# Optimization experiments

Hardware: AMD Instinct MI355X
Metric: run time of the kernel (lower is better)

Reference implementation:

```python
import jax, jax.numpy as jnp
import numpy as np

H = 132  # hidden size hard-coded in SpatialRelationLayer

def _mlp(x, w1, b1, w2, b2, w3, b3):
    # FCBlock: 2 hidden layers of width 132 with ReLU, then linear out;
    # NNNet wraps it with sigmoid(out * 5)
    h = jax.nn.relu(x @ w1 + b1)
    h = jax.nn.relu(h @ w2 + b2)
    return jax.nn.sigmoid((h @ w3 + b3) * 5.0)

def _mlp_params(key, din, dout):
    k1, k2, k3 = jax.random.split(key, 3)
    def lin(k, i, o):
        kw, kb = jax.random.split(k)
        s = 1.0 / np.sqrt(i)
        return (jax.random.uniform(kw, (i, o), jnp.float32, -s, s),
                jax.random.uniform(kb, (o,), jnp.float32, -s, s))
    w1, b1 = lin(k1, din, H)
    w2, b2 = lin(k2, H, H)
    w3, b3 = lin(k3, H, dout)
    return w1, b1, w2, b2, w3, b3

def setup_inputs() -> dict:
    key = jax.random.key(0)
    b, N, D0, D1, D2 = 8, 128, 128, 128, 64
    O0, O1, O2 = 64, 64, 64
    kP, kQ, kR, kp, kq, kr = jax.random.split(key, 6)
    inp = {
        "P": jax.random.normal(kP, (b, D0), jnp.float32),
        "Q": jax.random.normal(kQ, (b, N, D1), jnp.float32),
        "R": jax.random.normal(kR, (b, N, N, D2), jnp.float32),
    }
    for name, k, din, dout in (("p", kp, D0 + D1, O0),
                               ("q", kq, D1 + D0 + 2 * D2, O1),
                               ("r", kr, D2 + 2 * D1, O2)):
        w1, b1, w2, b2, w3, b3 = _mlp_params(k, din, dout)
        inp.update({f"{name}_w1": w1, f"{name}_b1": b1,
                    f"{name}_w2": w2, f"{name}_b2": b2,
                    f"{name}_w3": w3, f"{name}_b3": b3})
    return inp

def reference(P, Q, R,
              p_w1, p_b1, p_w2, p_b2, p_w3, p_b3,
              q_w1, q_b1, q_w2, q_b2, q_w3, q_b3,
              r_w1, r_b1, r_w2, r_b2, r_w3, r_b3):
    b, N, D1 = Q.shape
    # P branch: global max over objects, concat with P
    P_inputs = jnp.concatenate([jnp.max(Q, axis=1), P], axis=1)  # [b, D1+D0]
    P_out = _mlp(P_inputs, p_w1, p_b1, p_w2, p_b2, p_w3, p_b3)
    # Q branch: broadcast P per-object, max-reduce relations over each axis
    P_exp = jnp.broadcast_to(P[:, None, :], (b, N, P.shape[1]))  # [b,N,D0]
    R_red0 = jnp.max(R, axis=1)  # [b,N,D2]
    R_red1 = jnp.max(R, axis=2)  # [b,N,D2]
    Q_inputs = jnp.concatenate([P_exp, Q, R_red0, R_red1], axis=2)
    Q_out = _mlp(Q_inputs, q_w1, q_b1, q_w2, q_b2, q_w3, q_b3)
    # R branch: pairwise broadcast of Q along both axes, concat with R
    Q0 = jnp.broadcast_to(Q[:, None, :, :], (b, N, N, D1))  # repeat along dim 1
    Q1 = jnp.broadcast_to(Q[:, :, None, :], (b, N, N, D1))  # repeat along dim 2
    R_inputs = jnp.concatenate([R, Q0, Q1], axis=-1)  # [b,N,N,D2+2*D1]
    R_out = _mlp(R_inputs, r_w1, r_b1, r_w2, r_b2, r_w3, r_b3)
    return (P_out, Q_out, R_out)
```

## Files before the change

kernel.cpp:

```cpp
#include <hip/hip_runtime.h>

typedef _Float16 f16;
typedef f16 f16x8 __attribute__((ext_vector_type(8)));
typedef f16 f16x4 __attribute__((ext_vector_type(4)));
typedef float f32x4 __attribute__((ext_vector_type(4)));
typedef float f32x2 __attribute__((ext_vector_type(2)));

#define MFMA16(a, b, c) __builtin_amdgcn_mfma_f32_16x16x32_f16(a, b, c, 0, 0, 0)

#define OFF_RW1A 0
#define OFF_RW2  10240
#define OFF_RW3  35840
#define OFF_QW1  46080
#define OFF_QW2  87040
#define OFF_QW3  112640
#define OFF_PW1  122880
#define OFF_PW2  163840
#define OFF_PW3  189440
#define PACK_BYTES 399360

#define PREP_BLOCKS 1523

struct InPtrs { const float* p[21]; };

__device__ const int g_mSrc[9] = {15, 17, 19, 9, 11, 13, 3, 5, 7};
__device__ const int g_mK0[9]  = {0, 0, 0, 128, 0, 0, 0, 0, 0};
__device__ const int g_mK[9]   = {64, 132, 132, 256, 132, 132, 256, 132, 132};
__device__ const int g_mN[9]   = {132, 132, 64, 132, 132, 64, 132, 132, 64};
__device__ const int g_mNT[9]  = {10, 10, 4, 10, 10, 4, 10, 10, 4};
__device__ const int g_mDst[9] = {OFF_RW1A, OFF_RW2, OFF_RW3, OFF_QW1, OFF_QW2, OFF_QW3,
                                  OFF_PW1, OFF_PW2, OFF_PW3};
__device__ const int g_mBlk0[9] = {128, 133, 146, 151, 171, 184, 189, 209, 222};

__global__ __launch_bounds__(256) void prep_kernel(InPtrs in, f16* __restrict__ wpk,
    float* __restrict__ c1, float* __restrict__ d1, float* __restrict__ e1q,
    float* __restrict__ qmax, float* __restrict__ red0, float* __restrict__ red1)
{
  __shared__ float sbuf[1024];
  const int mb = blockIdx.x, t = threadIdx.x;

  if (mb < 128) {
    const int b = mb >> 4, jo = mb & 15;
    const float* base = in.p[2] + (size_t)b * 1048576 + (size_t)jo * 512 + t * 2;
    f32x2 m[8];
    #pragma unroll
    for (int u = 0; u < 8; ++u) { m[u][0] = -3.4e38f; m[u][1] = -3.4e38f; }
    for (int i = 0; i < 128; i += 8) {
      #pragma unroll
      for (int u = 0; u < 8; ++u) {
        f32x2 v = *(const f32x2*)(base + (size_t)(i + u) * 8192);
        m[u][0] = fmaxf(m[u][0], v[0]);
        m[u][1] = fmaxf(m[u][1], v[1]);
      }
    }
    #pragma unroll
    for (int s = 4; s > 0; s >>= 1)
      #pragma unroll
      for (int u = 0; u < 4; ++u)
        if (u < s) {
          m[u][0] = fmaxf(m[u][0], m[u + s][0]);
          m[u][1] = fmaxf(m[u][1], m[u + s][1]);
        }
    *(f32x2*)(red0 + ((size_t)(b * 128 + jo * 8 + (t >> 5))) * 64 + ((t * 2) & 63)) = m[0];
  } else if (mb < 227) {
    int mi = 8;
    while (mi > 0 && mb < g_mBlk0[mi]) --mi;
    const int NT = g_mNT[mi], K = g_mK[mi], N = g_mN[mi], K0 = g_mK0[mi];
    const int L = (mb - g_mBlk0[mi]) * 256 + t;
    const int lanes = ((K + 31) >> 5) * NT * 64;
    if (L < lanes) {
      const int lane = L & 63, tile = L >> 6;
      const int kk = tile / NT, nn = tile % NT;
      const float* src = in.p[g_mSrc[mi]];
      const int n = nn * 16 + (lane & 15);
      const int kb = kk * 32 + ((lane >> 4) << 3);
      f16x8 v;
      #pragma unroll
      for (int u = 0; u < 8; ++u) {
        const int k = kb + u;
        float f = (k < K && n < N) ? src[(size_t)(K0 + k) * N + n] : 0.f;
        v[u] = (f16)f;
      }
      *(f16x8*)(wpk + g_mDst[mi] + (size_t)L * 8) = v;
    }
  } else if (mb < 235) {
    const int b = mb - 227;
    const float* Qb = in.p[1] + (size_t)b * 128 * 128;
    const int d = t & 127, g = t >> 7;
    float m0 = -3.4e38f, m1 = m0, m2 = m0, m3 = m0;
    #pragma unroll
    for (int v = 0; v < 16; ++v) {
      const int i = g * 64 + v * 4;
      m0 = fmaxf(m0, Qb[(size_t)(i + 0) * 128 + d]);
      m1 = fmaxf(m1, Qb[(size_t)(i + 1) * 128 + d]);
      m2 = fmaxf(m2, Qb[(size_t)(i + 2) * 128 + d]);
      m3 = fmaxf(m3, Qb[(size_t)(i + 3) * 128 + d]);
    }
    sbuf[g * 128 + d] = fmaxf(fmaxf(m0, m1), fmaxf(m2, m3));
    __syncthreads();
    if (t < 128) qmax[b * 128 + t] = fmaxf(sbuf[t], sbuf[128 + t]);
  } else if (mb < 243) {
    const int b = mb - 235;
    const float* P = in.p[0]; const float* qw1 = in.p[9]; const float* qb1 = in.p[10];
    if (t < 160) {
      float a = 0.f;
      if (t < 132) {
        float a0 = 0.f, a1 = 0.f, a2 = 0.f, a3 = 0.f;
        for (int k = 0; k < 128; k += 4) {
          a0 += P[b * 128 + k + 0] * qw1[(size_t)(k + 0) * 132 + t];
          a1 += P[b * 128 + k + 1] * qw1[(size_t)(k + 1) * 132 + t];
          a2 += P[b * 128 + k + 2] * qw1[(size_t)(k + 2) * 132 + t];
          a3 += P[b * 128 + k + 3] * qw1[(size_t)(k + 3) * 132 + t];
        }
        a = qb1[t] + (a0 + a1) + (a2 + a3);
      }
      e1q[b * 160 + t] = a;
    }
  } else if (mb < 499) {
    const int blk = mb - 243;
    const float* Q = in.p[1]; const float* rw1 = in.p[15]; const float* rb1 = in.p[16];
    for (int o = t; o < 512; o += 256) sbuf[o] = Q[(size_t)blk * 512 + o];
    __syncthreads();
    if (t < 160) {
      float cc[4], dd[4];
      #pragma unroll
      for (int r = 0; r < 4; ++r) { cc[r] = 0.f; dd[r] = 0.f; }
      if (t < 132) {
        const float bb = rb1[t];
        #pragma unroll
        for (int r = 0; r < 4; ++r) cc[r] = bb;
        for (int k = 0; k < 128; ++k) {
          const float wc = rw1[(size_t)(192 + k) * 132 + t];
          const float wd = rw1[(size_t)(64 + k) * 132 + t];
          #pragma unroll
          for (int r = 0; r < 4; ++r) {
            cc[r] += sbuf[r * 128 + k] * wc;
            dd[r] += sbuf[r * 128 + k] * wd;
          }
        }
      }
      for (int r = 0; r < 4; ++r) {
        c1[(size_t)(blk * 4 + r) * 160 + t] = cc[r];
        d1[(size_t)(blk * 4 + r) * 160 + t] = dd[r];
      }
    }
  } else {
    const int bi = mb - 499;
    const int d2 = t & 31, jg = t >> 5;
    const float* base = in.p[2] + (size_t)bi * 8192 + (size_t)jg * 1024 + d2 * 2;
    f32x2 m[4];
    #pragma unroll
    for (int u = 0; u < 4; ++u) { m[u][0] = -3.4e38f; m[u][1] = -3.4e38f; }
    #pragma unroll
    for (int v = 0; v < 16; v += 4) {
      #pragma unroll
      for (int u = 0; u < 4; ++u) {
        f32x2 vv = *(const f32x2*)(base + (size_t)(v + u) * 64);
        m[u][0] = fmaxf(m[u][0], vv[0]);
        m[u][1] = fmaxf(m[u][1], vv[1]);
      }
    }
    m[0][0] = fmaxf(fmaxf(m[0][0], m[1][0]), fmaxf(m[2][0], m[3][0]));
    m[0][1] = fmaxf(fmaxf(m[0][1], m[1][1]), fmaxf(m[2][1], m[3][1]));
    sbuf[jg * 64 + d2 * 2] = m[0][0];
    sbuf[jg * 64 + d2 * 2 + 1] = m[0][1];
    __syncthreads();
    if (t < 64) {
      float mm = sbuf[t];
      #pragma unroll
      for (int g2 = 1; g2 < 8; ++g2) mm = fmaxf(mm, sbuf[g2 * 64 + t]);
      red1[(size_t)bi * 64 + t] = mm;
    }
  }
}

__device__ __forceinline__ float sig5(float x) {
  return 1.f / (1.f + __expf(-5.f * x));
}

__device__ __forceinline__ f16x8 ld_frag_f32(const float* p) {
  f32x4 v0 = *(const f32x4*)(p);
  f32x4 v1 = *(const f32x4*)(p + 4);
  f16x8 a;
  a[0] = (f16)v0[0]; a[1] = (f16)v0[1]; a[2] = (f16)v0[2]; a[3] = (f16)v0[3];
  a[4] = (f16)v1[0]; a[5] = (f16)v1[1]; a[6] = (f16)v1[2]; a[7] = (f16)v1[3];
  return a;
}

__global__ __launch_bounds__(256, 4) void fused_kernel(
    const float* __restrict__ R, const float* __restrict__ c1, const float* __restrict__ d1,
    const float* __restrict__ rb2, const float* __restrict__ rb3,
    const f16* __restrict__ wpk, float* __restrict__ outR,
    const float* __restrict__ P, const float* __restrict__ Q,
    const float* __restrict__ qb2, const float* __restrict__ qb3,
    const float* __restrict__ pb1, const float* __restrict__ pb2, const float* __restrict__ pb3,
    const float* __restrict__ e1q, const float* __restrict__ qmax,
    const float* __restrict__ red0, const float* __restrict__ red1,
    float* __restrict__ outP, float* __restrict__ outQ)
{
  __shared__ f16 Hs[64][168];
  const int blk = blockIdx.x;
  const int t = threadIdx.x, lane = t & 63, w = t >> 6;
  const int wm = w >> 1, wn = w & 1;
  const int lr = (lane >> 4) << 2;
  const int lc = lane & 15;
  const int lk = (lane >> 4) << 3;
  const int rbase = wm * 32, nbase = wn * 80;

  f32x4 acc[2][5];
  const float* b2p;
  const float* b3p;
  const f16x8* W2p;
  const f16x8* W3p;
  float* obase;
  int rowlim;

  if (blk >= 17) {
    const int idx = blk - 17;
    const int bi = idx >> 1, half = idx & 1;
    const int jbase = half * 64;
    const int b = bi >> 7;
    const float* Rb = R + (size_t)bi * 8192 + (size_t)jbase * 64;

    const float* c1r = c1 + (size_t)bi * 160;
    const float* d1b = d1 + ((size_t)b * 128 + jbase) * 160;
    f32x4 cvv[5];
    #pragma unroll
    for (int n5 = 0; n5 < 5; ++n5)
      cvv[n5] = *(const f32x4*)(c1r + nbase + n5 * 16 + lr);
    #pragma unroll
    for (int mi2 = 0; mi2 < 2; ++mi2) {
      const int jl = rbase + mi2 * 16 + lc;
      const float* dr = d1b + (size_t)jl * 160 + nbase + lr;
      #pragma unroll
      for (int n5 = 0; n5 < 5; ++n5)
        acc[mi2][n5] = cvv[n5] + *(const f32x4*)(dr + n5 * 16);
    }
    const f16x8* W1p = (const f16x8*)(wpk + OFF_RW1A);
    #pragma unroll
    for (int kk = 0; kk < 2; ++kk) {
      const f16x8 a0 = ld_frag_f32(Rb + (size_t)(rbase + lc) * 64 + kk * 32 + lk);
      const f16x8 a1 = ld_frag_f32(Rb + (size_t)(rbase + 16 + lc) * 64 + kk * 32 + lk);
      #pragma unroll
      for (int n5 = 0; n5 < 5; ++n5) {
        const f16x8 bf = W1p[(size_t)(kk * 10 + wn * 5 + n5) * 64 + lane];
        acc[0][n5] = MFMA16(bf, a0, acc[0][n5]);
        acc[1][n5] = MFMA16(bf, a1, acc[1][n5]);
      }
    }
    b2p = rb2; b3p = rb3;
    W2p = (const f16x8*)(wpk + OFF_RW2);
    W3p = (const f16x8*)(wpk + OFF_RW3);
    obase = outR + (size_t)bi * 8192 + (size_t)jbase * 64;
    rowlim = 64;
  } else {
    const int bs = blk;
    const bool isP = (bs == 16);
    const int b = bs >> 1, x0 = (bs & 1) * 64;
    const f16x8* W1p = (const f16x8*)(wpk + (isP ? OFF_PW1 : OFF_QW1));
    const f16x8 zz = {0, 0, 0, 0, 0, 0, 0, 0};

    #pragma unroll
    for (int n5 = 0; n5 < 5; ++n5) {
      const int nb = nbase + n5 * 16 + lr;
      f32x4 cv = {0.f, 0.f, 0.f, 0.f};
      if (isP) { if (nb < 132) cv = *(const f32x4*)(pb1 + nb); }
      else cv = *(const f32x4*)(e1q + b * 160 + nb);
      acc[0][n5] = cv; acc[1][n5] = cv;
    }
    for (int c = 0; c < 4; ++c) {
      #pragma unroll
      for (int kk = 0; kk < 2; ++kk) {
        const int kq = c * 64 + kk * 32 + lk;
        f16x8 a0 = zz, a1 = zz;
        if (isP) {
          #pragma unroll
          for (int mi2 = 0; mi2 < 2; ++mi2) {
            const int rl = rbase + mi2 * 16 + lc;
            f16x8 av = zz;
            if (rl < 8) {
              const float* s = (c < 2) ? (qmax + rl * 128 + kq) : (P + rl * 128 + (kq - 128));
              av = ld_frag_f32(s);
            }
            if (mi2 == 0) a0 = av; else a1 = av;
          }
        } else {
          #pragma unroll
          for (int mi2 = 0; mi2 < 2; ++mi2) {
            const size_t rg = (size_t)(b * 128 + x0 + rbase + mi2 * 16 + lc);
            const float* s = (c < 2) ? (Q + rg * 128 + kq)
                           : ((kq < 192) ? (red0 + rg * 64 + (kq - 128))
                                         : (red1 + rg * 64 + (kq - 192)));
            const f16x8 av = ld_frag_f32(s);
            if (mi2 == 0) a0 = av; else a1 = av;
          }
        }
        #pragma unroll
        for (int n5 = 0; n5 < 5; ++n5) {
          const f16x8 bf = W1p[(size_t)((c * 2 + kk) * 10 + wn * 5 + n5) * 64 + lane];
          acc[0][n5] = MFMA16(bf, a0, acc[0][n5]);
          acc[1][n5] = MFMA16(bf, a1, acc[1][n5]);
        }
      }
    }
    b2p = isP ? pb2 : qb2; b3p = isP ? pb3 : qb3;
    W2p = (const f16x8*)(wpk + (isP ? OFF_PW2 : OFF_QW2));
    W3p = (const f16x8*)(wpk + (isP ? OFF_PW3 : OFF_QW3));
    obase = isP ? outP : (outQ + ((size_t)(b * 128 + x0)) * 64);
    rowlim = isP ? 8 : 64;
  }

  #pragma unroll
  for (int mi2 = 0; mi2 < 2; ++mi2) {
    const int jl = rbase + mi2 * 16 + lc;
    #pragma unroll
    for (int n5 = 0; n5 < 5; ++n5) {
      f16x4 hv;
      #pragma unroll
      for (int r = 0; r < 4; ++r) hv[r] = (f16)fmaxf(acc[mi2][n5][r], 0.f);
      *(f16x4*)(&Hs[jl][nbase + n5 * 16 + lr]) = hv;
    }
  }
  __syncthreads();

  #pragma unroll
  for (int n5 = 0; n5 < 5; ++n5) {
    const int nb = nbase + n5 * 16 + lr;
    f32x4 bv = {0.f, 0.f, 0.f, 0.f};
    if (nb < 132) bv = *(const f32x4*)(b2p + nb);
    acc[0][n5] = bv; acc[1][n5] = bv;
  }
  #pragma unroll
  for (int kk = 0; kk < 5; ++kk) {
    const f16x8 a0 = *(const f16x8*)(&Hs[rbase + lc][kk * 32 + lk]);
    const f16x8 a1 = *(const f16x8*)(&Hs[rbase + 16 + lc][kk * 32 + lk]);
    #pragma unroll
    for (int n5 = 0; n5 < 5; ++n5) {
      const f16x8 bf = W2p[(size_t)(kk * 10 + wn * 5 + n5) * 64 + lane];
      acc[0][n5] = MFMA16(bf, a0, acc[0][n5]);
      acc[1][n5] = MFMA16(bf, a1, acc[1][n5]);
    }
  }
  __syncthreads();
  #pragma unroll
  for (int mi2 = 0; mi2 < 2; ++mi2) {
    const int jl = rbase + mi2 * 16 + lc;
    #pragma unroll
    for (int n5 = 0; n5 < 5; ++n5) {
      f16x4 hv;
      #pragma unroll
      for (int r = 0; r < 4; ++r) hv[r] = (f16)fmaxf(acc[mi2][n5][r], 0.f);
      *(f16x4*)(&Hs[jl][nbase + n5 * 16 + lr]) = hv;
    }
  }
  __syncthreads();

  f32x4 acc3[2][2];
  const int n3base = wn * 32;
  #pragma unroll
  for (int n2 = 0; n2 < 2; ++n2) {
    const f32x4 bv = *(const f32x4*)(b3p + n3base + n2 * 16 + lr);
    acc3[0][n2] = bv; acc3[1][n2] = bv;
  }
  #pragma unroll
  for (int kk = 0; kk < 5; ++kk) {
    const f16x8 a0 = *(const f16x8*)(&Hs[rbase + lc][kk * 32 + lk]);
    const f16x8 a1 = *(const f16x8*)(&Hs[rbase + 16 + lc][kk * 32 + lk]);
    #pragma unroll
    for (int n2 = 0; n2 < 2; ++n2) {
      const f16x8 bf = W3p[(size_t)(kk * 4 + wn * 2 + n2) * 64 + lane];
      acc3[0][n2] = MFMA16(bf, a0, acc3[0][n2]);
      acc3[1][n2] = MFMA16(bf, a1, acc3[1][n2]);
    }
  }
  #pragma unroll
  for (int mi2 = 0; mi2 < 2; ++mi2) {
    const int jl = rbase + mi2 * 16 + lc;
    if (jl < rowlim) {
      #pragma unroll
      for (int n2 = 0; n2 < 2; ++n2) {
        f32x4 ov;
        #pragma unroll
        for (int r = 0; r < 4; ++r) ov[r] = sig5(acc3[mi2][n2][r]);
        *(f32x4*)(obase + (size_t)jl * 64 + n3base + n2 * 16 + lr) = ov;
      }
    }
  }
}

extern "C" void kernel_launch(void* const* d_in, const int* in_sizes, int n_in,
                              void* d_out, int out_size, void* d_ws, size_t ws_size,
                              hipStream_t stream) {
  (void)in_sizes; (void)n_in; (void)out_size; (void)ws_size;
  InPtrs ip;
  for (int i = 0; i < 21; ++i) ip.p[i] = (const float*)d_in[i];

  char* ws = (char*)d_ws;
  f16* wpk = (f16*)ws;
  float* wsf = (float*)(ws + PACK_BYTES);
  float* c1 = wsf;
  float* d1 = wsf + 163840;
  float* e1q = wsf + 327680;
  float* qmax = wsf + 328960;
  float* red0 = wsf + 329984;
  float* red1 = wsf + 395520;

  float* outP = (float*)d_out;
  float* outQ = outP + 512;
  float* outR = outP + 66048;

  prep_kernel<<<dim3(PREP_BLOCKS), dim3(256), 0, stream>>>(ip, wpk, c1, d1, e1q, qmax, red0, red1);
  fused_kernel<<<dim3(2065), dim3(256), 0, stream>>>((const float*)d_in[2], c1, d1,
      (const float*)d_in[18], (const float*)d_in[20], wpk, outR,
      (const float*)d_in[0], (const float*)d_in[1],
      (const float*)d_in[12], (const float*)d_in[14],
      (const float*)d_in[4], (const float*)d_in[6], (const float*)d_in[8],
      e1q, qmax, red0, red1, outP, outQ);
}
```

Measured before the change: 64.46 us.

## Make each wave own full MLP rows and pass hidden layers via lane shuffles

The fused MLP kernel now gives each wave 32 rows across all 132 hidden columns, so layer outputs are repacked into MFMA operand fragments with cross-lane shuffles instead of going through shared memory and __syncthreads. It also uses packed round-to-zero f16 conversion, splits the R max-over-axis-1 reduction into two halves combined in the Q branch, and relaxes launch bounds to 3 blocks. The aim is to remove LDS traffic and block barriers and to add parallelism to the column reduction. In exchange, register pressure rises from doubled accumulators and there are extra shuffle instructions.

```diff
diff --git a/kernel.cpp b/kernel.cpp
--- a/kernel.cpp
+++ b/kernel.cpp
@@ -2,9 +2,9 @@
 
 typedef _Float16 f16;
 typedef f16 f16x8 __attribute__((ext_vector_type(8)));
-typedef f16 f16x4 __attribute__((ext_vector_type(4)));
 typedef float f32x4 __attribute__((ext_vector_type(4)));
 typedef float f32x2 __attribute__((ext_vector_type(2)));
+typedef unsigned u32;
 
 #define MFMA16(a, b, c) __builtin_amdgcn_mfma_f32_16x16x32_f16(a, b, c, 0, 0, 0)
 
@@ -19,7 +19,7 @@
 #define OFF_PW3  189440
 #define PACK_BYTES 399360
 
-#define PREP_BLOCKS 1523
+#define PREP_BLOCKS 1651
 
 struct InPtrs { const float* p[21]; };
 
@@ -30,22 +30,23 @@
 __device__ const int g_mNT[9]  = {10, 10, 4, 10, 10, 4, 10, 10, 4};
 __device__ const int g_mDst[9] = {OFF_RW1A, OFF_RW2, OFF_RW3, OFF_QW1, OFF_QW2, OFF_QW3,
                                   OFF_PW1, OFF_PW2, OFF_PW3};
-__device__ const int g_mBlk0[9] = {128, 133, 146, 151, 171, 184, 189, 209, 222};
+__device__ const int g_mBlk0[9] = {256, 261, 274, 279, 299, 312, 317, 337, 350};
 
 __global__ __launch_bounds__(256) void prep_kernel(InPtrs in, f16* __restrict__ wpk,
     float* __restrict__ c1, float* __restrict__ d1, float* __restrict__ e1q,
-    float* __restrict__ qmax, float* __restrict__ red0, float* __restrict__ red1)
+    float* __restrict__ qmax, float* __restrict__ red0p, float* __restrict__ red1)
 {
   __shared__ float sbuf[1024];
   const int mb = blockIdx.x, t = threadIdx.x;
 
-  if (mb < 128) {
-    const int b = mb >> 4, jo = mb & 15;
-    const float* base = in.p[2] + (size_t)b * 1048576 + (size_t)jo * 512 + t * 2;
+  if (mb < 256) {
+    const int b = mb >> 5, jo = (mb >> 1) & 15, ih = mb & 1;
+    const float* base = in.p[2] + (size_t)b * 1048576 + (size_t)ih * 64 * 8192
+                        + (size_t)jo * 512 + t * 2;
     f32x2 m[8];
     #pragma unroll
     for (int u = 0; u < 8; ++u) { m[u][0] = -3.4e38f; m[u][1] = -3.4e38f; }
-    for (int i = 0; i < 128; i += 8) {
+    for (int i = 0; i < 64; i += 8) {
       #pragma unroll
       for (int u = 0; u < 8; ++u) {
         f32x2 v = *(const f32x2*)(base + (size_t)(i + u) * 8192);
@@ -61,8 +62,9 @@
           m[u][0] = fmaxf(m[u][0], m[u + s][0]);
           m[u][1] = fmaxf(m[u][1], m[u + s][1]);
         }
-    *(f32x2*)(red0 + ((size_t)(b * 128 + jo * 8 + (t >> 5))) * 64 + ((t * 2) & 63)) = m[0];
-  } else if (mb < 227) {
+    *(f32x2*)(red0p + (size_t)ih * 65536 +
+              ((size_t)(b * 128 + jo * 8 + (t >> 5))) * 64 + ((t * 2) & 63)) = m[0];
+  } else if (mb < 355) {
     int mi = 8;
     while (mi > 0 && mb < g_mBlk0[mi]) --mi;
     const int NT = g_mNT[mi], K = g_mK[mi], N = g_mN[mi], K0 = g_mK0[mi];
@@ -83,8 +85,8 @@
       }
       *(f16x8*)(wpk + g_mDst[mi] + (size_t)L * 8) = v;
     }
-  } else if (mb < 235) {
-    const int b = mb - 227;
+  } else if (mb < 363) {
+    const int b = mb - 355;
     const float* Qb = in.p[1] + (size_t)b * 128 * 128;
     const int d = t & 127, g = t >> 7;
     float m0 = -3.4e38f, m1 = m0, m2 = m0, m3 = m0;
@@ -99,8 +101,8 @@
     sbuf[g * 128 + d] = fmaxf(fmaxf(m0, m1), fmaxf(m2, m3));
     __syncthreads();
     if (t < 128) qmax[b * 128 + t] = fmaxf(sbuf[t], sbuf[128 + t]);
-  } else if (mb < 243) {
-    const int b = mb - 235;
+  } else if (mb < 371) {
+    const int b = mb - 363;
     const float* P = in.p[0]; const float* qw1 = in.p[9]; const float* qb1 = in.p[10];
     if (t < 160) {
       float a = 0.f;
@@ -116,8 +118,8 @@
       }
       e1q[b * 160 + t] = a;
     }
-  } else if (mb < 499) {
-    const int blk = mb - 243;
+  } else if (mb < 627) {
+    const int blk = mb - 371;
     const float* Q = in.p[1]; const float* rw1 = in.p[15]; const float* rb1 = in.p[16];
     for (int o = t; o < 512; o += 256) sbuf[o] = Q[(size_t)blk * 512 + o];
     __syncthreads();
@@ -145,7 +147,7 @@
       }
     }
   } else {
-    const int bi = mb - 499;
+    const int bi = mb - 627;
     const int d2 = t & 31, jg = t >> 5;
     const float* base = in.p[2] + (size_t)bi * 8192 + (size_t)jg * 1024 + d2 * 2;
     f32x2 m[4];
@@ -178,16 +180,51 @@
   return 1.f / (1.f + __expf(-5.f * x));
 }
 
-__device__ __forceinline__ f16x8 ld_frag_f32(const float* p) {
-  f32x4 v0 = *(const f32x4*)(p);
-  f32x4 v1 = *(const f32x4*)(p + 4);
-  f16x8 a;
-  a[0] = (f16)v0[0]; a[1] = (f16)v0[1]; a[2] = (f16)v0[2]; a[3] = (f16)v0[3];
-  a[4] = (f16)v1[0]; a[5] = (f16)v1[1]; a[6] = (f16)v1[2]; a[7] = (f16)v1[3];
-  return a;
-}
-
-__global__ __launch_bounds__(256, 4) void fused_kernel(
+__device__ __forceinline__ u32 pk2(float a, float b) {
+  typedef __fp16 fp16x2 __attribute__((ext_vector_type(2)));
+  union { fp16x2 h; u32 u; } cv;
+  cv.h = __builtin_amdgcn_cvt_pkrtz(a, b);
+  return cv.u;
+}
+
+__device__ __forceinline__ f16x8 ld8(const float* p) {
+  f32x4 v0 = *(const f32x4*)p, v1 = *(const f32x4*)(p + 4);
+  union { u32 w[4]; f16x8 v; } U;
+  U.w[0] = pk2(v0[0], v0[1]); U.w[1] = pk2(v0[2], v0[3]);
+  U.w[2] = pk2(v1[0], v1[1]); U.w[3] = pk2(v1[2], v1[3]);
+  return U.v;
+}
+
+__device__ __forceinline__ f16x8 ld8max(const float* p, int stride) {
+  f32x4 a0 = *(const f32x4*)p, a1 = *(const f32x4*)(p + 4);
+  f32x4 b0 = *(const f32x4*)(p + stride), b1 = *(const f32x4*)(p + stride + 4);
+  union { u32 w[4]; f16x8 v; } U;
+  U.w[0] = pk2(fmaxf(a0[0], b0[0]), fmaxf(a0[1], b0[1]));
+  U.w[1] = pk2(fmaxf(a0[2], b0[2]), fmaxf(a0[3], b0[3]));
+  U.w[2] = pk2(fmaxf(a1[0], b1[0]), fmaxf(a1[1], b1[1]));
+  U.w[3] = pk2(fmaxf(a1[2], b1[2]), fmaxf(a1[3], b1[3]));
+  return U.v;
+}
+
+__device__ __forceinline__ f16x8 make_bfrag(const f32x4 ta, const f32x4 tb,
+                                            int srcA, int srcB, bool glo) {
+  u32 a0 = pk2(fmaxf(ta[0], 0.f), fmaxf(ta[1], 0.f));
+  u32 a1 = pk2(fmaxf(ta[2], 0.f), fmaxf(ta[3], 0.f));
+  u32 b0 = pk2(fmaxf(tb[0], 0.f), fmaxf(tb[1], 0.f));
+  u32 b1 = pk2(fmaxf(tb[2], 0.f), fmaxf(tb[3], 0.f));
+  u32 aA0 = (u32)__shfl((int)a0, srcA), aA1 = (u32)__shfl((int)a1, srcA);
+  u32 bA0 = (u32)__shfl((int)b0, srcA), bA1 = (u32)__shfl((int)b1, srcA);
+  u32 aB0 = (u32)__shfl((int)a0, srcB), aB1 = (u32)__shfl((int)a1, srcB);
+  u32 bB0 = (u32)__shfl((int)b0, srcB), bB1 = (u32)__shfl((int)b1, srcB);
+  union { u32 w[4]; f16x8 v; } U;
+  U.w[0] = glo ? aA0 : bA0;
+  U.w[1] = glo ? aA1 : bA1;
+  U.w[2] = glo ? aB0 : bB0;
+  U.w[3] = glo ? aB1 : bB1;
+  return U.v;
+}
+
+__global__ __launch_bounds__(256, 3) void fused_kernel(
     const float* __restrict__ R, const float* __restrict__ c1, const float* __restrict__ d1,
     const float* __restrict__ rb2, const float* __restrict__ rb3,
     const f16* __restrict__ wpk, float* __restrict__ outR,
@@ -195,194 +232,170 @@
     const float* __restrict__ qb2, const float* __restrict__ qb3,
     const float* __restrict__ pb1, const float* __restrict__ pb2, const float* __restrict__ pb3,
     const float* __restrict__ e1q, const float* __restrict__ qmax,
-    const float* __restrict__ red0, const float* __restrict__ red1,
+    const float* __restrict__ red0p, const float* __restrict__ red1,
     float* __restrict__ outP, float* __restrict__ outQ)
 {
-  __shared__ f16 Hs[64][168];
-  const int blk = blockIdx.x;
   const int t = threadIdx.x, lane = t & 63, w = t >> 6;
-  const int wm = w >> 1, wn = w & 1;
-  const int lr = (lane >> 4) << 2;
-  const int lc = lane & 15;
-  const int lk = (lane >> 4) << 3;
-  const int rbase = wm * 32, nbase = wn * 80;
-
-  f32x4 acc[2][5];
-  const float* b2p;
-  const float* b3p;
-  const f16x8* W2p;
-  const f16x8* W3p;
+  const int g = lane >> 4, i = lane & 15;
+  const int nrow = g * 4;
+  const bool glo = (g < 2);
+  const int srcA = ((2 * g) & 3) * 16 + i;
+  const int srcB = ((2 * g + 1) & 3) * 16 + i;
+  const int wv = blockIdx.x * 4 + w;
+  if (wv >= 4129) return;
+
+  f32x4 acc[2][10];
+  const f16x8 *W2p, *W3p;
+  const float *b2p, *b3p;
   float* obase;
   int rowlim;
 
-  if (blk >= 17) {
-    const int idx = blk - 17;
-    const int bi = idx >> 1, half = idx & 1;
-    const int jbase = half * 64;
+  if (wv >= 33) {
+    const int widx = wv - 33;
+    const int bi = widx >> 2, rowbase = (widx & 3) * 32;
     const int b = bi >> 7;
-    const float* Rb = R + (size_t)bi * 8192 + (size_t)jbase * 64;
-
     const float* c1r = c1 + (size_t)bi * 160;
-    const float* d1b = d1 + ((size_t)b * 128 + jbase) * 160;
-    f32x4 cvv[5];
-    #pragma unroll
-    for (int n5 = 0; n5 < 5; ++n5)
-      cvv[n5] = *(const f32x4*)(c1r + nbase + n5 * 16 + lr);
-    #pragma unroll
-    for (int mi2 = 0; mi2 < 2; ++mi2) {
-      const int jl = rbase + mi2 * 16 + lc;
-      const float* dr = d1b + (size_t)jl * 160 + nbase + lr;
-      #pragma unroll
-      for (int n5 = 0; n5 < 5; ++n5)
-        acc[mi2][n5] = cvv[n5] + *(const f32x4*)(dr + n5 * 16);
+    const float* d1b = d1 + ((size_t)(b * 128 + rowbase)) * 160;
+    #pragma unroll
+    for (int tn = 0; tn < 10; ++tn) {
+      const f32x4 cv = *(const f32x4*)(c1r + tn * 16 + nrow);
+      #pragma unroll
+      for (int tj = 0; tj < 2; ++tj)
+        acc[tj][tn] = cv + *(const f32x4*)(d1b + (size_t)(tj * 16 + i) * 160 + tn * 16 + nrow);
     }
     const f16x8* W1p = (const f16x8*)(wpk + OFF_RW1A);
-    #pragma unroll
-    for (int kk = 0; kk < 2; ++kk) {
-      const f16x8 a0 = ld_frag_f32(Rb + (size_t)(rbase + lc) * 64 + kk * 32 + lk);
-      const f16x8 a1 = ld_frag_f32(Rb + (size_t)(rbase + 16 + lc) * 64 + kk * 32 + lk);
-      #pragma unroll
-      for (int n5 = 0; n5 < 5; ++n5) {
-        const f16x8 bf = W1p[(size_t)(kk * 10 + wn * 5 + n5) * 64 + lane];
-        acc[0][n5] = MFMA16(bf, a0, acc[0][n5]);
-        acc[1][n5] = MFMA16(bf, a1, acc[1][n5]);
-      }
-    }
+    const float* Rb = R + (size_t)bi * 8192 + (size_t)rowbase * 64;
+    #pragma unroll
+    for (int c = 0; c < 2; ++c) {
+      const f16x8 x0 = ld8(Rb + (size_t)i * 64 + c * 32 + g * 8);
+      const f16x8 x1 = ld8(Rb + (size_t)(16 + i) * 64 + c * 32 + g * 8);
+      #pragma unroll
+      for (int tn = 0; tn < 10; ++tn) {
+        const f16x8 bf = W1p[(size_t)(c * 10 + tn) * 64 + lane];
+        acc[0][tn] = MFMA16(bf, x0, acc[0][tn]);
+        acc[1][tn] = MFMA16(bf, x1, acc[1][tn]);
+      }
+    }
+    W2p = (const f16x8*)(wpk + OFF_RW2); W3p = (const f16x8*)(wpk + OFF_RW3);
     b2p = rb2; b3p = rb3;
-    W2p = (const f16x8*)(wpk + OFF_RW2);
-    W3p = (const f16x8*)(wpk + OFF_RW3);
-    obase = outR + (size_t)bi * 8192 + (size_t)jbase * 64;
-    rowlim = 64;
+    obase = outR + (size_t)bi * 8192 + (size_t)rowbase * 64;
+    rowlim = 32;
+  } else if (wv < 32) {
+    const int b = wv >> 2, rowbase = (wv & 3) * 32;
+    const int rgb = b * 128 + rowbase;
+    #pragma unroll
+    for (int tn = 0; tn < 10; ++tn) {
+      const f32x4 ev = *(const f32x4*)(e1q + b * 160 + tn * 16 + nrow);
+      acc[0][tn] = ev; acc[1][tn] = ev;
+    }
+    const f16x8* W1p = (const f16x8*)(wpk + OFF_QW1);
+    #pragma unroll
+    for (int c = 0; c < 8; ++c) {
+      f16x8 x[2];
+      #pragma unroll
+      for (int tj = 0; tj < 2; ++tj) {
+        const size_t row = (size_t)(rgb + tj * 16 + i);
+        if (c < 4)      x[tj] = ld8(Q + row * 128 + c * 32 + g * 8);
+        else if (c < 6) x[tj] = ld8max(red0p + row * 64 + (c - 4) * 32 + g * 8, 65536);
+        else            x[tj] = ld8(red1 + row * 64 + (c - 6) * 32 + g * 8);
+      }
+      #pragma unroll
+      for (int tn = 0; tn < 10; ++tn) {
+        const f16x8 bf = W1p[(size_t)(c * 10 + tn) * 64 + lane];
+        acc[0][tn] = MFMA16(bf, x[0], acc[0][tn]);
+        acc[1][tn] = MFMA16(bf, x[1], acc[1][tn]);
+      }
+    }
+    W2p = (const f16x8*)(wpk + OFF_QW2); W3p = (const f16x8*)(wpk + OFF_QW3);
+    b2p = qb2; b3p = qb3;
+    obase = outQ + (size_t)rgb * 64;
+    rowlim = 32;
   } else {
-    const int bs = blk;
-    const bool isP = (bs == 16);
-    const int b = bs >> 1, x0 = (bs & 1) * 64;
-    const f16x8* W1p = (const f16x8*)(wpk + (isP ? OFF_PW1 : OFF_QW1));
-    const f16x8 zz = {0, 0, 0, 0, 0, 0, 0, 0};
-
-    #pragma unroll
-    for (int n5 = 0; n5 < 5; ++n5) {
-      const int nb = nbase + n5 * 16 + lr;
+    #pragma unroll
+    for (int tn = 0; tn < 10; ++tn) {
+      const int nb = tn * 16 + nrow;
       f32x4 cv = {0.f, 0.f, 0.f, 0.f};
-      if (isP) { if (nb < 132) cv = *(const f32x4*)(pb1 + nb); }
-      else cv = *(const f32x4*)(e1q + b * 160 + nb);
-      acc[0][n5] = cv; acc[1][n5] = cv;
-    }
-    for (int c = 0; c < 4; ++c) {
-      #pragma unroll
-      for (int kk = 0; kk < 2; ++kk) {
-        const int kq = c * 64 + kk * 32 + lk;
-        f16x8 a0 = zz, a1 = zz;
-        if (isP) {
-          #pragma unroll
-          for (int mi2 = 0; mi2 < 2; ++mi2) {
-            const int rl = rbase + mi2 * 16 + lc;
-            f16x8 av = zz;
-            if (rl < 8) {
-              const float* s = (c < 2) ? (qmax + rl * 128 + kq) : (P + rl * 128 + (kq - 128));
-              av = ld_frag_f32(s);
-            }
-            if (mi2 == 0) a0 = av; else a1 = av;
-          }
-        } else {
-          #pragma unroll
-          for (int mi2 = 0; mi2 < 2; ++mi2) {
-            const size_t rg = (size_t)(b * 128 + x0 + rbase + mi2 * 16 + lc);
-            const float* s = (c < 2) ? (Q + rg * 128 + kq)
-                           : ((kq < 192) ? (red0 + rg * 64 + (kq - 128))
-                                         : (red1 + rg * 64 + (kq - 192)));
-            const f16x8 av = ld_frag_f32(s);
-            if (mi2 == 0) a0 = av; else a1 = av;
-          }
-        }
-        #pragma unroll
-        for (int n5 = 0; n5 < 5; ++n5) {
-          const f16x8 bf = W1p[(size_t)((c * 2 + kk) * 10 + wn * 5 + n5) * 64 + lane];
-          acc[0][n5] = MFMA16(bf, a0, acc[0][n5]);
-          acc[1][n5] = MFMA16(bf, a1, acc[1][n5]);
-        }
-      }
-    }
-    b2p = isP ? pb2 : qb2; b3p = isP ? pb3 : qb3;
-    W2p = (const f16x8*)(wpk + (isP ? OFF_PW2 : OFF_QW2));
-    W3p = (const f16x8*)(wpk + (isP ? OFF_PW3 : OFF_QW3));
-    obase = isP ? outP : (outQ + ((size_t)(b * 128 + x0)) * 64);
-    rowlim = isP ? 8 : 64;
+      if (nb < 132) cv = *(const f32x4*)(pb1 + nb);
+      acc[0][tn] = cv; acc[1][tn] = cv;
+    }
+    const f16x8* W1p = (const f16x8*)(wpk + OFF_PW1);
+    #pragma unroll
+    for (int c = 0; c < 8; ++c) {
+      f16x8 x[2];
+      #pragma unroll
+      for (int tj = 0; tj < 2; ++tj) {
+        const int rr = (tj * 16 + i) & 7;
+        const float* s = (c < 4) ? (qmax + rr * 128 + c * 32 + g * 8)
+                                 : (P + rr * 128 + (c - 4) * 32 + g * 8);
+        x[tj] = ld8(s);
+      }
+      #pragma unroll
+      for (int tn = 0; tn < 10; ++tn) {
+        const f16x8 bf = W1p[(size_t)(c * 10 + tn) * 64 + lane];
+        acc[0][tn] = MFMA16(bf, x[0], acc[0][tn]);
+        acc[1][tn] = MFMA16(bf, x[1], acc[1][tn]);
+      }
+    }
+    W2p = (const f16x8*)(wpk + OFF_PW2); W3p = (const f16x8*)(wpk + OFF_PW3);
+    b2p = pb2; b3p = pb3;
+    obase = outP;
+    rowlim = 8;
   }
 
-  #pragma unroll
-  for (int mi2 = 0; mi2 < 2; ++mi2) {
-    const int jl = rbase + mi2 * 16 + lc;
-    #pragma unroll
-    for (int n5 = 0; n5 < 5; ++n5) {
-      f16x4 hv;
-      #pragma unroll
-      for (int r = 0; r < 4; ++r) hv[r] = (f16)fmaxf(acc[mi2][n5][r], 0.f);
-      *(f16x4*)(&Hs[jl][nbase + n5 * 16 + lr]) = hv;
-    }
-  }
-  __syncthreads();
-
-  #pragma unroll
-  for (int n5 = 0; n5 < 5; ++n5) {
-    const int nb = nbase + n5 * 16 + lr;
+  f16x8 hf[5][2];
+  #pragma unroll
+  for (int c = 0; c < 5; ++c)
+    #pragma unroll
+    for (int tj = 0; tj < 2; ++tj)
+      hf[c][tj] = make_bfrag(acc[tj][2 * c], acc[tj][2 * c + 1], srcA, srcB, glo);
+
+  #pragma unroll
+  for (int tn = 0; tn < 10; ++tn) {
+    const int nb = tn * 16 + nrow;
     f32x4 bv = {0.f, 0.f, 0.f, 0.f};
     if (nb < 132) bv = *(const f32x4*)(b2p + nb);
-    acc[0][n5] = bv; acc[1][n5] = bv;
+    acc[0][tn] = bv; acc[1][tn] = bv;
   }
   #pragma unroll
-  for (int kk = 0; kk < 5; ++kk) {
-    const f16x8 a0 = *(const f16x8*)(&Hs[rbase + lc][kk * 32 + lk]);
-    const f16x8 a1 = *(const f16x8*)(&Hs[rbase + 16 + lc][kk * 32 + lk]);
-    #pragma unroll
-    for (int n5 = 0; n5 < 5; ++n5) {
-      const f16x8 bf = W2p[(size_t)(kk * 10 + wn * 5 + n5) * 64 + lane];
-      acc[0][n5] = MFMA16(bf, a0, acc[0][n5]);
-      acc[1][n5] = MFMA16(bf, a1, acc[1][n5]);
-    }
+  for (int c = 0; c < 5; ++c)
+    #pragma unroll
+    for (int tn = 0; tn < 10; ++tn) {
+      const f16x8 bf = W2p[(size_t)(c * 10 + tn) * 64 + lane];
+      acc[0][tn] = MFMA16(bf, hf[c][0], acc[0][tn]);
+      acc[1][tn] = MFMA16(bf, hf[c][1], acc[1][tn]);
+    }
+
+  #pragma unroll
+  for (int c = 0; c < 5; ++c)
+    #pragma unroll
+    for (int tj = 0; tj < 2; ++tj)
+      hf[c][tj] = make_bfrag(acc[tj][2 * c], acc[tj][2 * c + 1], srcA, srcB, glo);
+
+  f32x4 a3[2][4];
+  #pragma unroll
+  for (int tn = 0; tn < 4; ++tn) {
+    const f32x4 bv = *(const f32x4*)(b3p + tn * 16 + nrow);
+    a3[0][tn] = bv; a3[1][tn] = bv;
   }
-  __syncthreads();
-  #pragma unroll
-  for (int mi2 = 0; mi2 < 2; ++mi2) {
-    const int jl = rbase + mi2 * 16 + lc;
-    #pragma unroll
-    for (int n5 = 0; n5 < 5; ++n5) {
-      f16x4 hv;
-      #pragma unroll
-      for (int r = 0; r < 4; ++r) hv[r] = (f16)fmaxf(acc[mi2][n5][r], 0.f);
-      *(f16x4*)(&Hs[jl][nbase + n5 * 16 + lr]) = hv;
-    }
-  }
-  __syncthreads();
-
-  f32x4 acc3[2][2];
-  const int n3base = wn * 32;
-  #pragma unroll
-  for (int n2 = 0; n2 < 2; ++n2) {
-    const f32x4 bv = *(const f32x4*)(b3p + n3base + n2 * 16 + lr);
-    acc3[0][n2] = bv; acc3[1][n2] = bv;
-  }
-  #pragma unroll
-  for (int kk = 0; kk < 5; ++kk) {
-    const f16x8 a0 = *(const f16x8*)(&Hs[rbase + lc][kk * 32 + lk]);
-    const f16x8 a1 = *(const f16x8*)(&Hs[rbase + 16 + lc][kk * 32 + lk]);
-    #pragma unroll
-    for (int n2 = 0; n2 < 2; ++n2) {
-      const f16x8 bf = W3p[(size_t)(kk * 4 + wn * 2 + n2) * 64 + lane];
-      acc3[0][n2] = MFMA16(bf, a0, acc3[0][n2]);
-      acc3[1][n2] = MFMA16(bf, a1, acc3[1][n2]);
-    }
-  }
-  #pragma unroll
-  for (int mi2 = 0; mi2 < 2; ++mi2) {
-    const int jl = rbase + mi2 * 16 + lc;
-    if (jl < rowlim) {
-      #pragma unroll
-      for (int n2 = 0; n2 < 2; ++n2) {
+  #pragma unroll
+  for (int c = 0; c < 5; ++c)
+    #pragma unroll
+    for (int tn = 0; tn < 4; ++tn) {
+      const f16x8 bf = W3p[(size_t)(c * 4 + tn) * 64 + lane];
+      a3[0][tn] = MFMA16(bf, hf[c][0], a3[0][tn]);
+      a3[1][tn] = MFMA16(bf, hf[c][1], a3[1][tn]);
+    }
+
+  #pragma unroll
+  for (int tj = 0; tj < 2; ++tj) {
+    const int jr = tj * 16 + i;
+    if (jr < rowlim) {
+      #pragma unroll
+      for (int tn = 0; tn < 4; ++tn) {
         f32x4 ov;
         #pragma unroll
-        for (int r = 0; r < 4; ++r) ov[r] = sig5(acc3[mi2][n2][r]);
-        *(f32x4*)(obase + (size_t)jl * 64 + n3base + n2 * 16 + lr) = ov;
+        for (int r = 0; r < 4; ++r) ov[r] = sig5(a3[tj][tn][r]);
+        *(f32x4*)(obase + (size_t)jr * 64 + tn * 16 + nrow) = ov;
       }
     }
   }
@@ -402,18 +415,19 @@
   float* d1 = wsf + 163840;
   float* e1q = wsf + 327680;
   float* qmax = wsf + 328960;
-  float* red0 = wsf + 329984;
-  float* red1 = wsf + 395520;
+  float* red0p = wsf + 329984;
+  float* red1 = wsf + 461056;
 
   float* outP = (float*)d_out;
   float* outQ = outP + 512;
   float* outR = outP + 66048;
 
-  prep_kernel<<<dim3(PREP_BLOCKS), dim3(256), 0, stream>>>(ip, wpk, c1, d1, e1q, qmax, red0, red1);
-  fused_kernel<<<dim3(2065), dim3(256), 0, stream>>>((const float*)d_in[2], c1, d1,
+  prep_kernel<<<dim3(PREP_BLOCKS), dim3(256), 0, stream>>>(ip, wpk, c1, d1, e1q, qmax,
+                                                           red0p, red1);
+  fused_kernel<<<dim3(1033), dim3(256), 0, stream>>>((const float*)d_in[2], c1, d1,
       (const float*)d_in[18], (const float*)d_in[20], wpk, outR,
       (const float*)d_in[0], (const float*)d_in[1],
       (const float*)d_in[12], (const float*)d_in[14],
       (const float*)d_in[4], (const float*)d_in[6], (const float*)d_in[8],
-      e1q, qmax, red0, red1, outP, outQ);
-}
+      e1q, qmax, red0p, red1, outP, outQ);
+}
```

Result: slower. 83.23 us (+29.1%).

## Split R column-max into two halves and use 512-thread fused blocks

Applied to the files above, without the earlier changes.

The axis-1 max over R in the prep kernel is split into two half-range blocks that write partial maxima, and the Q branch combines the two partials while loading. The fused kernel now uses 512-thread blocks that each cover a full 128-row tile instead of two 64-row halves, which halves the block count and shares bias/weight setup. The fp32-to-fp16 fragment conversion switches to packed cvt_pkrtz, which changes rounding from nearest to toward-zero. The extra partial buffer adds workspace and a second load in the Q branch. The larger blocks may reduce occupancy because LDS use doubles.

```diff
diff --git a/kernel.cpp b/kernel.cpp
--- a/kernel.cpp
+++ b/kernel.cpp
@@ -5,6 +5,7 @@
 typedef f16 f16x4 __attribute__((ext_vector_type(4)));
 typedef float f32x4 __attribute__((ext_vector_type(4)));
 typedef float f32x2 __attribute__((ext_vector_type(2)));
+typedef unsigned u32;
 
 #define MFMA16(a, b, c) __builtin_amdgcn_mfma_f32_16x16x32_f16(a, b, c, 0, 0, 0)
 
@@ -19,7 +20,7 @@
 #define OFF_PW3  189440
 #define PACK_BYTES 399360
 
-#define PREP_BLOCKS 1523
+#define PREP_BLOCKS 1651
 
 struct InPtrs { const float* p[21]; };
 
@@ -30,22 +31,23 @@
 __device__ const int g_mNT[9]  = {10, 10, 4, 10, 10, 4, 10, 10, 4};
 __device__ const int g_mDst[9] = {OFF_RW1A, OFF_RW2, OFF_RW3, OFF_QW1, OFF_QW2, OFF_QW3,
                                   OFF_PW1, OFF_PW2, OFF_PW3};
-__device__ const int g_mBlk0[9] = {128, 133, 146, 151, 171, 184, 189, 209, 222};
+__device__ const int g_mBlk0[9] = {256, 261, 274, 279, 299, 312, 317, 337, 350};
 
 __global__ __launch_bounds__(256) void prep_kernel(InPtrs in, f16* __restrict__ wpk,
     float* __restrict__ c1, float* __restrict__ d1, float* __restrict__ e1q,
-    float* __restrict__ qmax, float* __restrict__ red0, float* __restrict__ red1)
+    float* __restrict__ qmax, float* __restrict__ red0p, float* __restrict__ red1)
 {
   __shared__ float sbuf[1024];
   const int mb = blockIdx.x, t = threadIdx.x;
 
-  if (mb < 128) {
-    const int b = mb >> 4, jo = mb & 15;
-    const float* base = in.p[2] + (size_t)b * 1048576 + (size_t)jo * 512 + t * 2;
+  if (mb < 256) {
+    const int b = mb >> 5, jo = (mb >> 1) & 15, ih = mb & 1;
+    const float* base = in.p[2] + (size_t)b * 1048576 + (size_t)ih * 64 * 8192
+                        + (size_t)jo * 512 + t * 2;
     f32x2 m[8];
     #pragma unroll
     for (int u = 0; u < 8; ++u) { m[u][0] = -3.4e38f; m[u][1] = -3.4e38f; }
-    for (int i = 0; i < 128; i += 8) {
+    for (int i = 0; i < 64; i += 8) {
       #pragma unroll
       for (int u = 0; u < 8; ++u) {
         f32x2 v = *(const f32x2*)(base + (size_t)(i + u) * 8192);
@@ -61,8 +63,9 @@
           m[u][0] = fmaxf(m[u][0], m[u + s][0]);
           m[u][1] = fmaxf(m[u][1], m[u + s][1]);
         }
-    *(f32x2*)(red0 + ((size_t)(b * 128 + jo * 8 + (t >> 5))) * 64 + ((t * 2) & 63)) = m[0];
-  } else if (mb < 227) {
+    *(f32x2*)(red0p + (size_t)ih * 65536 +
+              ((size_t)(b * 128 + jo * 8 + (t >> 5))) * 64 + ((t * 2) & 63)) = m[0];
+  } else if (mb < 355) {
     int mi = 8;
     while (mi > 0 && mb < g_mBlk0[mi]) --mi;
     const int NT = g_mNT[mi], K = g_mK[mi], N = g_mN[mi], K0 = g_mK0[mi];
@@ -83,8 +86,8 @@
       }
       *(f16x8*)(wpk + g_mDst[mi] + (size_t)L * 8) = v;
     }
-  } else if (mb < 235) {
-    const int b = mb - 227;
+  } else if (mb < 363) {
+    const int b = mb - 355;
     const float* Qb = in.p[1] + (size_t)b * 128 * 128;
     const int d = t & 127, g = t >> 7;
     float m0 = -3.4e38f, m1 = m0, m2 = m0, m3 = m0;
@@ -99,8 +102,8 @@
     sbuf[g * 128 + d] = fmaxf(fmaxf(m0, m1), fmaxf(m2, m3));
     __syncthreads();
     if (t < 128) qmax[b * 128 + t] = fmaxf(sbuf[t], sbuf[128 + t]);
-  } else if (mb < 243) {
-    const int b = mb - 235;
+  } else if (mb < 371) {
+    const int b = mb - 363;
     const float* P = in.p[0]; const float* qw1 = in.p[9]; const float* qb1 = in.p[10];
     if (t < 160) {
       float a = 0.f;
@@ -116,8 +119,8 @@
       }
       e1q[b * 160 + t] = a;
     }
-  } else if (mb < 499) {
-    const int blk = mb - 243;
+  } else if (mb < 627) {
+    const int blk = mb - 371;
     const float* Q = in.p[1]; const float* rw1 = in.p[15]; const float* rb1 = in.p[16];
     for (int o = t; o < 512; o += 256) sbuf[o] = Q[(size_t)blk * 512 + o];
     __syncthreads();
@@ -145,7 +148,7 @@
       }
     }
   } else {
-    const int bi = mb - 499;
+    const int bi = mb - 627;
     const int d2 = t & 31, jg = t >> 5;
     const float* base = in.p[2] + (size_t)bi * 8192 + (size_t)jg * 1024 + d2 * 2;
     f32x2 m[4];
@@ -178,16 +181,33 @@
   return 1.f / (1.f + __expf(-5.f * x));
 }
 
-__device__ __forceinline__ f16x8 ld_frag_f32(const float* p) {
-  f32x4 v0 = *(const f32x4*)(p);
-  f32x4 v1 = *(const f32x4*)(p + 4);
-  f16x8 a;
-  a[0] = (f16)v0[0]; a[1] = (f16)v0[1]; a[2] = (f16)v0[2]; a[3] = (f16)v0[3];
-  a[4] = (f16)v1[0]; a[5] = (f16)v1[1]; a[6] = (f16)v1[2]; a[7] = (f16)v1[3];
-  return a;
-}
-
-__global__ __launch_bounds__(256, 4) void fused_kernel(
+__device__ __forceinline__ u32 pk2(float a, float b) {
+  typedef __fp16 fp16x2 __attribute__((ext_vector_type(2)));
+  union { fp16x2 h; u32 u; } cv;
+  cv.h = __builtin_amdgcn_cvt_pkrtz(a, b);
+  return cv.u;
+}
+
+__device__ __forceinline__ f16x8 ld8(const float* p) {
+  f32x4 v0 = *(const f32x4*)p, v1 = *(const f32x4*)(p + 4);
+  union { u32 w[4]; f16x8 v; } U;
+  U.w[0] = pk2(v0[0], v0[1]); U.w[1] = pk2(v0[2], v0[3]);
+  U.w[2] = pk2(v1[0], v1[1]); U.w[3] = pk2(v1[2], v1[3]);
+  return U.v;
+}
+
+__device__ __forceinline__ f16x8 ld8max(const float* p, int stride) {
+  f32x4 a0 = *(const f32x4*)p, a1 = *(const f32x4*)(p + 4);
+  f32x4 b0 = *(const f32x4*)(p + stride), b1 = *(const f32x4*)(p + stride + 4);
+  union { u32 w[4]; f16x8 v; } U;
+  U.w[0] = pk2(fmaxf(a0[0], b0[0]), fmaxf(a0[1], b0[1]));
+  U.w[1] = pk2(fmaxf(a0[2], b0[2]), fmaxf(a0[3], b0[3]));
+  U.w[2] = pk2(fmaxf(a1[0], b1[0]), fmaxf(a1[1], b1[1]));
+  U.w[3] = pk2(fmaxf(a1[2], b1[2]), fmaxf(a1[3], b1[3]));
+  return U.v;
+}
+
+__global__ __launch_bounds__(512, 4) void fused_kernel(
     const float* __restrict__ R, const float* __restrict__ c1, const float* __restrict__ d1,
     const float* __restrict__ rb2, const float* __restrict__ rb3,
     const f16* __restrict__ wpk, float* __restrict__ outR,
@@ -195,35 +215,29 @@
     const float* __restrict__ qb2, const float* __restrict__ qb3,
     const float* __restrict__ pb1, const float* __restrict__ pb2, const float* __restrict__ pb3,
     const float* __restrict__ e1q, const float* __restrict__ qmax,
-    const float* __restrict__ red0, const float* __restrict__ red1,
+    const float* __restrict__ red0p, const float* __restrict__ red1,
     float* __restrict__ outP, float* __restrict__ outQ)
 {
-  __shared__ f16 Hs[64][168];
-  const int blk = blockIdx.x;
+  __shared__ f16 Hs[128][168];
   const int t = threadIdx.x, lane = t & 63, w = t >> 6;
   const int wm = w >> 1, wn = w & 1;
   const int lr = (lane >> 4) << 2;
   const int lc = lane & 15;
   const int lk = (lane >> 4) << 3;
   const int rbase = wm * 32, nbase = wn * 80;
+  const int blk = blockIdx.x;
 
   f32x4 acc[2][5];
-  const float* b2p;
-  const float* b3p;
-  const f16x8* W2p;
-  const f16x8* W3p;
+  const f16x8 *W2p, *W3p;
+  const float *b2p, *b3p;
   float* obase;
   int rowlim;
 
-  if (blk >= 17) {
-    const int idx = blk - 17;
-    const int bi = idx >> 1, half = idx & 1;
-    const int jbase = half * 64;
+  if (blk >= 9) {
+    const int bi = blk - 9;
     const int b = bi >> 7;
-    const float* Rb = R + (size_t)bi * 8192 + (size_t)jbase * 64;
-
     const float* c1r = c1 + (size_t)bi * 160;
-    const float* d1b = d1 + ((size_t)b * 128 + jbase) * 160;
+    const float* d1b = d1 + (size_t)b * 128 * 160;
     f32x4 cvv[5];
     #pragma unroll
     for (int n5 = 0; n5 < 5; ++n5)
@@ -237,13 +251,14 @@
         acc[mi2][n5] = cvv[n5] + *(const f32x4*)(dr + n5 * 16);
     }
     const f16x8* W1p = (const f16x8*)(wpk + OFF_RW1A);
-    #pragma unroll
-    for (int kk = 0; kk < 2; ++kk) {
-      const f16x8 a0 = ld_frag_f32(Rb + (size_t)(rbase + lc) * 64 + kk * 32 + lk);
-      const f16x8 a1 = ld_frag_f32(Rb + (size_t)(rbase + 16 + lc) * 64 + kk * 32 + lk);
+    const float* Rb = R + (size_t)bi * 8192;
+    #pragma unroll
+    for (int c = 0; c < 2; ++c) {
+      const f16x8 a0 = ld8(Rb + (size_t)(rbase + lc) * 64 + c * 32 + lk);
+      const f16x8 a1 = ld8(Rb + (size_t)(rbase + 16 + lc) * 64 + c * 32 + lk);
       #pragma unroll
       for (int n5 = 0; n5 < 5; ++n5) {
-        const f16x8 bf = W1p[(size_t)(kk * 10 + wn * 5 + n5) * 64 + lane];
+        const f16x8 bf = W1p[(size_t)(c * 10 + wn * 5 + n5) * 64 + lane];
         acc[0][n5] = MFMA16(bf, a0, acc[0][n5]);
         acc[1][n5] = MFMA16(bf, a1, acc[1][n5]);
       }
@@ -251,15 +266,11 @@
     b2p = rb2; b3p = rb3;
     W2p = (const f16x8*)(wpk + OFF_RW2);
     W3p = (const f16x8*)(wpk + OFF_RW3);
-    obase = outR + (size_t)bi * 8192 + (size_t)jbase * 64;
-    rowlim = 64;
+    obase = outR + (size_t)bi * 8192;
+    rowlim = 128;
   } else {
-    const int bs = blk;
-    const bool isP = (bs == 16);
-    const int b = bs >> 1, x0 = (bs & 1) * 64;
-    const f16x8* W1p = (const f16x8*)(wpk + (isP ? OFF_PW1 : OFF_QW1));
-    const f16x8 zz = {0, 0, 0, 0, 0, 0, 0, 0};
-
+    const bool isP = (blk == 8);
+    const int b = blk;
     #pragma unroll
     for (int n5 = 0; n5 < 5; ++n5) {
       const int nb = nbase + n5 * 16 + lr;
@@ -268,46 +279,37 @@
       else cv = *(const f32x4*)(e1q + b * 160 + nb);
       acc[0][n5] = cv; acc[1][n5] = cv;
     }
-    for (int c = 0; c < 4; ++c) {
-      #pragma unroll
-      for (int kk = 0; kk < 2; ++kk) {
-        const int kq = c * 64 + kk * 32 + lk;
-        f16x8 a0 = zz, a1 = zz;
+    const f16x8* W1p = (const f16x8*)(wpk + (isP ? OFF_PW1 : OFF_QW1));
+    #pragma unroll
+    for (int c = 0; c < 8; ++c) {
+      f16x8 x[2];
+      #pragma unroll
+      for (int mi2 = 0; mi2 < 2; ++mi2) {
+        const int jl = rbase + mi2 * 16 + lc;
         if (isP) {
-          #pragma unroll
-          for (int mi2 = 0; mi2 < 2; ++mi2) {
-            const int rl = rbase + mi2 * 16 + lc;
-            f16x8 av = zz;
-            if (rl < 8) {
-              const float* s = (c < 2) ? (qmax + rl * 128 + kq) : (P + rl * 128 + (kq - 128));
-              av = ld_frag_f32(s);
-            }
-            if (mi2 == 0) a0 = av; else a1 = av;
-          }
+          const int rr = jl & 7;
+          const float* s = (c < 4) ? (qmax + rr * 128 + c * 32 + lk)
+                                   : (P + rr * 128 + (c - 4) * 32 + lk);
+          x[mi2] = ld8(s);
         } else {
-          #pragma unroll
-          for (int mi2 = 0; mi2 < 2; ++mi2) {
-            const size_t rg = (size_t)(b * 128 + x0 + rbase + mi2 * 16 + lc);
-            const float* s = (c < 2) ? (Q + rg * 128 + kq)
-                           : ((kq < 192) ? (red0 + rg * 64 + (kq - 128))
-                                         : (red1 + rg * 64 + (kq - 192)));
-            const f16x8 av = ld_frag_f32(s);
-            if (mi2 == 0) a0 = av; else a1 = av;
-          }
+          const size_t row = (size_t)(b * 128 + jl);
+          if (c < 4)      x[mi2] = ld8(Q + row * 128 + c * 32 + lk);
+          else if (c < 6) x[mi2] = ld8max(red0p + row * 64 + (c - 4) * 32 + lk, 65536);
+          else            x[mi2] = ld8(red1 + row * 64 + (c - 6) * 32 + lk);
         }
-        #pragma unroll
-        for (int n5 = 0; n5 < 5; ++n5) {
-          const f16x8 bf = W1p[(size_t)((c * 2 + kk) * 10 + wn * 5 + n5) * 64 + lane];
-          acc[0][n5] = MFMA16(bf, a0, acc[0][n5]);
-          acc[1][n5] = MFMA16(bf, a1, acc[1][n5]);
-        }
+      }
+      #pragma unroll
+      for (int n5 = 0; n5 < 5; ++n5) {
+        const f16x8 bf = W1p[(size_t)(c * 10 + wn * 5 + n5) * 64 + lane];
+        acc[0][n5] = MFMA16(bf, x[0], acc[0][n5]);
+        acc[1][n5] = MFMA16(bf, x[1], acc[1][n5]);
       }
     }
     b2p = isP ? pb2 : qb2; b3p = isP ? pb3 : qb3;
     W2p = (const f16x8*)(wpk + (isP ? OFF_PW2 : OFF_QW2));
     W3p = (const f16x8*)(wpk + (isP ? OFF_PW3 : OFF_QW3));
-    obase = isP ? outP : (outQ + ((size_t)(b * 128 + x0)) * 64);
-    rowlim = isP ? 8 : 64;
+    obase = isP ? outP : (outQ + (size_t)b * 128 * 64);
+    rowlim = isP ? 8 : 128;
   }
 
   #pragma unroll
@@ -402,18 +404,19 @@
   float* d1 = wsf + 163840;
   float* e1q = wsf + 327680;
   float* qmax = wsf + 328960;
-  float* red0 = wsf + 329984;
-  float* red1 = wsf + 395520;
+  float* red0p = wsf + 329984;
+  float* red1 = wsf + 461056;
 
   float* outP = (float*)d_out;
   float* outQ = outP + 512;
   float* outR = outP + 66048;
 
-  prep_kernel<<<dim3(PREP_BLOCKS), dim3(256), 0, stream>>>(ip, wpk, c1, d1, e1q, qmax, red0, red1);
-  fused_kernel<<<dim3(2065), dim3(256), 0, stream>>>((const float*)d_in[2], c1, d1,
+  prep_kernel<<<dim3(PREP_BLOCKS), dim3(256), 0, stream>>>(ip, wpk, c1, d1, e1q, qmax,
+                                                           red0p, red1);
+  fused_kernel<<<dim3(1033), dim3(512), 0, stream>>>((const float*)d_in[2], c1, d1,
       (const float*)d_in[18], (const float*)d_in[20], wpk, outR,
       (const float*)d_in[0], (const float*)d_in[1],
       (const float*)d_in[12], (const float*)d_in[14],
       (const float*)d_in[4], (const float*)d_in[6], (const float*)d_in[8],
-      e1q, qmax, red0, red1, outP, outQ);
-}
+      e1q, qmax, red0p, red1, outP, outQ);
+}
```

New measurement: 69.50 us. 7.8% more time.
